# Kernel optimization log

Hardware: AMD Instinct MI355X
Metric: run time of the kernel (lower is better)

The kernel has to match this reference:

```python
import jax, jax.numpy as jnp
import numpy as np

N_NODES = 50000
N_EDGES = 1600000
IN_CH = 512
HID = 8      # per-head features, layer 1
HEADS = 8
OUT_CH = 40  # num classes
NEG_SLOPE = 0.2  # PyG GATConv default leaky_relu slope


def setup_inputs() -> dict:
    key = jax.random.key(0)
    ks = jax.random.split(key, 8)
    x = jax.random.uniform(ks[0], (N_NODES, IN_CH), dtype=jnp.float32)
    edge_index = jax.random.randint(ks[1], (2, N_EDGES), 0, N_NODES, dtype=jnp.int64)
    s1 = 1.0 / np.sqrt(IN_CH)
    s2 = 1.0 / np.sqrt(HEADS * HID)
    W1 = jax.random.normal(ks[2], (IN_CH, HEADS * HID), dtype=jnp.float32) * s1
    att_src1 = jax.random.normal(ks[3], (HEADS, HID), dtype=jnp.float32) * s2
    att_dst1 = jax.random.normal(ks[4], (HEADS, HID), dtype=jnp.float32) * s2
    b1 = jnp.zeros((HEADS * HID,), dtype=jnp.float32)
    W2 = jax.random.normal(ks[5], (HEADS * HID, OUT_CH), dtype=jnp.float32) * s2
    att_src2 = jax.random.normal(ks[6], (1, OUT_CH), dtype=jnp.float32) * 0.15
    att_dst2 = jax.random.normal(ks[7], (1, OUT_CH), dtype=jnp.float32) * 0.15
    b2 = jnp.zeros((OUT_CH,), dtype=jnp.float32)
    return {"x": x, "edge_index": edge_index, "W1": W1, "att_src1": att_src1,
            "att_dst1": att_dst1, "b1": b1, "W2": W2, "att_src2": att_src2,
            "att_dst2": att_dst2, "b2": b2}


def _row_normalize(x):
    return x / jnp.clip(x.sum(axis=1, keepdims=True), 1e-8, None)


def _gat_conv(x, src, dst, W, att_src, att_dst, bias, heads, out_ch, concat):
    """PyG GATConv (self-loops already included in src/dst)."""
    n = x.shape[0]
    h = (x @ W).reshape(n, heads, out_ch)          # [N, H, C]
    a_src = jnp.sum(h * att_src, axis=-1)          # [N, H]
    a_dst = jnp.sum(h * att_dst, axis=-1)          # [N, H]
    alpha = jax.nn.leaky_relu(a_src[src] + a_dst[dst], NEG_SLOPE)  # [E, H]
    # segment softmax over incoming edges of each dst node
    m = jax.ops.segment_max(alpha, dst, num_segments=n)            # [N, H]
    e = jnp.exp(alpha - m[dst])
    denom = jax.ops.segment_sum(e, dst, num_segments=n)            # [N, H]
    alpha = e / (denom[dst] + 1e-16)
    msg = h[src] * alpha[:, :, None]               # [E, H, C]
    out = jax.ops.segment_sum(msg, dst, num_segments=n)            # [N, H, C]
    out = out.reshape(n, heads * out_ch) if concat else out.mean(axis=1)
    return out + bias


def reference(x, edge_index, W1, att_src1, att_dst1, b1, W2, att_src2, att_dst2, b2):
    n = x.shape[0]
    loops = jnp.arange(n, dtype=edge_index.dtype)
    src = jnp.concatenate([edge_index[0], loops])
    dst = jnp.concatenate([edge_index[1], loops])
    h = _row_normalize(x)
    # dropout omitted: inference mode (training=False)
    h = jax.nn.elu(_gat_conv(h, src, dst, W1, att_src1, att_dst1, b1, HEADS, HID, True))
    return _gat_conv(h, src, dst, W2, att_src2, att_dst2, b2, 1, OUT_CH, False)
```

## Files before the change

### kernel.cpp

```cpp
#include <hip/hip_runtime.h>
#include <math.h>

#define N_NODES 50000
#define IN_CH   512
#define HID     8
#define HEADS   8
#define C1      64
#define OUT_CH  40
#define NEG_SLOPE 0.2f
#define NB      ((N_NODES + 255) / 256)
#define TILE    4096
#define CAP     16384

__device__ __forceinline__ float leaky(float v) { return fmaxf(v, NEG_SLOPE * v); }
__device__ __forceinline__ float fexp(float v) { return __expf(v); }

typedef __attribute__((ext_vector_type(8))) short short8;
typedef __attribute__((ext_vector_type(4))) short short4v;
typedef __attribute__((ext_vector_type(4))) float f32x4;

__device__ __forceinline__ unsigned short f2bf(float f) {
    unsigned u = __builtin_bit_cast(unsigned, f);
    u += 0x7FFFu + ((u >> 16) & 1u);
    return (unsigned short)(u >> 16);
}
__device__ __forceinline__ float bf2f(unsigned short h) {
    unsigned u = ((unsigned)h) << 16;
    return __builtin_bit_cast(float, u);
}

#define XH_STRIDE_B 272

__global__ __launch_bounds__(256) void k_packW(
    const float* __restrict__ W1, short* __restrict__ bph, short* __restrict__ bpl)
{
    const int idx = blockIdx.x * 256 + threadIdx.x;
    if (idx >= 512 * 64) return;
    const int k = idx >> 6, col = idx & 63;
    const float w = W1[idx];
    const unsigned short hi = f2bf(w);
    const unsigned short lo = f2bf(w - bf2f(hi));
    const int di = ((k >> 5) * 64 + col) * 32 + (k & 31);
    bph[di] = (short)hi;
    bpl[di] = (short)lo;
}

__global__ __launch_bounds__(256) void k_gemm1_mfma(
    const float* __restrict__ x,
    const short* __restrict__ bph, const short* __restrict__ bpl,
    const float* __restrict__ attS, const float* __restrict__ attD,
    unsigned short* __restrict__ h1b, float* __restrict__ aS, float* __restrict__ aD)
{
    __shared__ unsigned char smem[17536];
    short* xh = (short*)smem;
    short* xl = (short*)(smem + 8704);
    float* rowsum = (float*)(smem + 17408);
    float* houtf  = (float*)smem;

    const int tid  = threadIdx.x;
    const int lane = tid & 63;
    const int w    = tid >> 6;
    const int row_off = (w & 1) * 16;
    const int col_off = (w >> 1) * 32;
    const int rowBase = blockIdx.x * 32;

    const int l15 = lane & 15;
    const int kg  = lane >> 4;
    const int a_base = (l15 + row_off) * XH_STRIDE_B + kg * 16;

    const int srow = tid >> 5;
    const int sk4  = tid & 31;

    f32x4 acc0 = {0.f, 0.f, 0.f, 0.f};
    f32x4 acc1 = {0.f, 0.f, 0.f, 0.f};
    float psum[4] = {0.f, 0.f, 0.f, 0.f};
    float4 va[4], vb[4];

    auto LOAD = [&](int c, float4 (&v)[4]) {
        #pragma unroll
        for (int i = 0; i < 4; ++i) {
            const int grow = rowBase + i * 8 + srow;
            v[i] = (grow < N_NODES)
                 ? *(const float4*)(x + (size_t)grow * IN_CH + c * 128 + sk4 * 4)
                 : make_float4(0.f, 0.f, 0.f, 0.f);
        }
    };
    auto STAGE = [&](float4 (&v)[4]) {
        #pragma unroll
        for (int i = 0; i < 4; ++i) {
            const int row = i * 8 + srow;
            const unsigned short h0 = f2bf(v[i].x), h1u = f2bf(v[i].y),
                                 h2 = f2bf(v[i].z), h3  = f2bf(v[i].w);
            short4v hvv = { (short)h0, (short)h1u, (short)h2, (short)h3 };
            short4v lvv = { (short)f2bf(v[i].x - bf2f(h0)), (short)f2bf(v[i].y - bf2f(h1u)),
                            (short)f2bf(v[i].z - bf2f(h2)), (short)f2bf(v[i].w - bf2f(h3)) };
            *(short4v*)((char*)xh + row * XH_STRIDE_B + sk4 * 8) = hvv;
            *(short4v*)((char*)xl + row * XH_STRIDE_B + sk4 * 8) = lvv;
            psum[i] += v[i].x + v[i].y + v[i].z + v[i].w;
        }
    };
    auto MFMA = [&](int c) {
        #pragma unroll
        for (int kk2 = 0; kk2 < 4; ++kk2) {
            const int kk = c * 4 + kk2;
            const short8 ah = *(const short8*)((const char*)xh + a_base + kk2 * 64);
            const short8 al = *(const short8*)((const char*)xl + a_base + kk2 * 64);
            const int b0 = (kk * 64 + col_off + l15) * 32 + kg * 8;
            const int b1 = b0 + 16 * 32;
            const short8 bh0 = *(const short8*)(bph + b0);
            const short8 bl0 = *(const short8*)(bpl + b0);
            const short8 bh1 = *(const short8*)(bph + b1);
            const short8 bl1 = *(const short8*)(bpl + b1);
            acc0 = __builtin_amdgcn_mfma_f32_16x16x32_bf16(ah, bh0, acc0, 0, 0, 0);
            acc1 = __builtin_amdgcn_mfma_f32_16x16x32_bf16(ah, bh1, acc1, 0, 0, 0);
            acc0 = __builtin_amdgcn_mfma_f32_16x16x32_bf16(ah, bl0, acc0, 0, 0, 0);
            acc1 = __builtin_amdgcn_mfma_f32_16x16x32_bf16(ah, bl1, acc1, 0, 0, 0);
            acc0 = __builtin_amdgcn_mfma_f32_16x16x32_bf16(al, bh0, acc0, 0, 0, 0);
            acc1 = __builtin_amdgcn_mfma_f32_16x16x32_bf16(al, bh1, acc1, 0, 0, 0);
        }
    };

    LOAD(0, va);
    STAGE(va);
    __syncthreads();
    LOAD(1, vb);
    MFMA(0);
    __syncthreads();
    STAGE(vb);
    __syncthreads();
    LOAD(2, va);
    MFMA(1);
    __syncthreads();
    STAGE(va);
    __syncthreads();
    LOAD(3, vb);
    MFMA(2);
    __syncthreads();
    STAGE(vb);
    #pragma unroll
    for (int i = 0; i < 4; ++i) {
        float s = psum[i];
        #pragma unroll
        for (int off = 16; off; off >>= 1) s += __shfl_xor(s, off, 32);
        if (sk4 == 0) rowsum[i * 8 + srow] = s;
    }
    __syncthreads();
    MFMA(3);
    __syncthreads();

    #pragma unroll
    for (int r = 0; r < 4; ++r) {
        const int row = row_off + kg * 4 + r;
        const float rs = fmaxf(rowsum[row], 1e-8f);
        houtf[row * 68 + col_off + l15]      = acc0[r] / rs;
        houtf[row * 68 + col_off + 16 + l15] = acc1[r] / rs;
    }
    __syncthreads();

    #pragma unroll
    for (int i = tid; i < 32 * 16; i += 256) {
        const int row = i >> 4, seg = i & 15;
        if (rowBase + row < N_NODES) {
            const float* hs = houtf + row * 68 + seg * 4;
            short4v o = { (short)f2bf(hs[0]), (short)f2bf(hs[1]),
                          (short)f2bf(hs[2]), (short)f2bf(hs[3]) };
            *(short4v*)(h1b + (size_t)(rowBase + row) * 64 + seg * 4) = o;
        }
    }

    {
        const int row = tid >> 3, hd = tid & 7;
        if (rowBase + row < N_NODES) {
            float vs = 0.f, vd = 0.f;
            #pragma unroll
            for (int e2 = 0; e2 < 8; ++e2) {
                const float hv = houtf[row * 68 + hd * 8 + e2];
                vs = fmaf(hv, attS[hd * 8 + e2], vs);
                vd = fmaf(hv, attD[hd * 8 + e2], vd);
            }
            aS[(size_t)(rowBase + row) * 8 + hd] = vs;
            aD[(size_t)(rowBase + row) * 8 + hd] = vd;
        }
    }
}

__global__ __launch_bounds__(256) void k_initCur(int* __restrict__ coarseCur)
{
    const int t = threadIdx.x;
    if (t < NB) coarseCur[t] = t * CAP;
}

__global__ __launch_bounds__(256) void k_part(
    const int* __restrict__ src, const int* __restrict__ dst, int E,
    int* __restrict__ coarseCur, unsigned int* __restrict__ pairs)
{
    __shared__ int  hist[256];
    __shared__ int  scn[256];
    __shared__ int  offs[256];
    __shared__ unsigned int  pairBuf[TILE];
    __shared__ unsigned char bktBuf[TILE];

    const int t = threadIdx.x;
    const int tileBase = blockIdx.x * TILE;
    const int n = min(TILE, E - tileBase);

    hist[t] = 0;
    __syncthreads();

    for (int e = t; e < n; e += 256)
        atomicAdd(&hist[dst[tileBase + e] >> 8], 1);
    __syncthreads();

    scn[t] = hist[t];
    __syncthreads();
    #pragma unroll
    for (int off = 1; off < 256; off <<= 1) {
        int xv = (t >= off) ? scn[t - off] : 0;
        __syncthreads();
        scn[t] += xv;
        __syncthreads();
    }

    {
        const int h  = hist[t];
        const int ls = scn[t] - h;
        int off = 0;
        if (h > 0) {
            const int gbase = atomicAdd(&coarseCur[t], h);
            off = gbase - ls;
        }
        offs[t] = off;
        hist[t] = ls;
    }
    __syncthreads();

    for (int e = t; e < n; e += 256) {
        const int s = src[tileBase + e];
        const int d = dst[tileBase + e];
        const int bkt = d >> 8;
        const int pos = atomicAdd(&hist[bkt], 1);
        pairBuf[pos] = (unsigned)s | ((unsigned)(d & 255) << 17);
        bktBuf[pos]  = (unsigned char)bkt;
    }
    __syncthreads();

    for (int i = t; i < n; i += 256)
        pairs[i + offs[bktBuf[i]]] = pairBuf[i];
}

__global__ __launch_bounds__(256) void k_fine2(
    const int* __restrict__ coarseCur,
    const unsigned int* __restrict__ pairs, int* __restrict__ ssrc,
    int* __restrict__ cumS, int* __restrict__ cumE)
{
    __shared__ int hist[256];
    __shared__ int scn[256];
    __shared__ int cur[256];
    const int b = blockIdx.x;
    const int t = threadIdx.x;
    const int dbase = b << 8;
    const int nd = min(256, N_NODES - dbase);
    const int lo = b * CAP;
    const int hi = coarseCur[b];

    hist[t] = 0;
    __syncthreads();
    for (int j = lo + t; j < hi; j += 256)
        atomicAdd(&hist[(pairs[j] >> 17) & 255], 1);
    __syncthreads();

    const int hv = hist[t];
    scn[t] = hv;
    __syncthreads();
    #pragma unroll
    for (int off = 1; off < 256; off <<= 1) {
        int xv = (t >= off) ? scn[t - off] : 0;
        __syncthreads();
        scn[t] += xv;
        __syncthreads();
    }
    if (t < nd) {
        cumS[dbase + t] = lo + scn[t] - hv;
        cumE[dbase + t] = lo + scn[t];
    }
    cur[t] = lo + scn[t] - hv;
    __syncthreads();

    for (int j = lo + t; j < hi; j += 256) {
        const unsigned int p = pairs[j];
        const int pos = atomicAdd(&cur[(p >> 17) & 255], 1);
        ssrc[pos] = (int)(p & 0x1FFFFu);
    }
}

__global__ __launch_bounds__(256) void k_agg1f(
    const int* __restrict__ cumS, const int* __restrict__ cumE,
    const int* __restrict__ ssrc,
    const float* __restrict__ aS, const float* __restrict__ aD,
    const unsigned short* __restrict__ h1b, const float* __restrict__ b1,
    const float* __restrict__ W2,
    const float* __restrict__ attS2, const float* __restrict__ attD2,
    unsigned short* __restrict__ h2b, float* __restrict__ a2s, float* __restrict__ a2d)
{
    __shared__ float w2s[64 * 40];
    __shared__ float hstage[4][64];

    const int tid  = threadIdx.x;
    const int lane = tid & 63;
    const int w    = tid >> 6;
    const int node = __builtin_amdgcn_readfirstlane(blockIdx.x * 4 + w);
    const int e = lane >> 3;
    const int c = lane & 7;

    #pragma unroll
    for (int i = tid; i < 640; i += 256)
        ((float4*)w2s)[i] = ((const float4*)W2)[i];

    const int start = cumS[node];
    const int end   = cumE[node];

    const float aDn = aD[(size_t)node * 8 + c];
    float acc[8] = {0.f, 0.f, 0.f, 0.f, 0.f, 0.f, 0.f, 0.f};
    float den = 0.f;

    if (e == 0) {
        const float e0 = fexp(leaky(aS[(size_t)node * 8 + c] + aDn));
        const short8 hv = *(const short8*)(h1b + (size_t)node * 64 + c * 8);
        #pragma unroll
        for (int j = 0; j < 8; ++j)
            acc[j] = e0 * bf2f((unsigned short)hv[j]);
        den = e0;
    }

    int base = start;
    for (; base + 32 <= end; base += 32) {
        const int s0 = ssrc[base + e];
        const int s1 = ssrc[base + 8 + e];
        const int s2 = ssrc[base + 16 + e];
        const int s3 = ssrc[base + 24 + e];
        const float aa0 = aS[(size_t)s0 * 8 + c];
        const float aa1 = aS[(size_t)s1 * 8 + c];
        const float aa2 = aS[(size_t)s2 * 8 + c];
        const float aa3 = aS[(size_t)s3 * 8 + c];
        const short8 h0 = *(const short8*)(h1b + ((size_t)s0 << 6) + c * 8);
        const short8 h1v = *(const short8*)(h1b + ((size_t)s1 << 6) + c * 8);
        const short8 h2v = *(const short8*)(h1b + ((size_t)s2 << 6) + c * 8);
        const short8 h3v = *(const short8*)(h1b + ((size_t)s3 << 6) + c * 8);
        const float w0 = fexp(leaky(aa0 + aDn));
        const float w1 = fexp(leaky(aa1 + aDn));
        const float w2 = fexp(leaky(aa2 + aDn));
        const float w3 = fexp(leaky(aa3 + aDn));
        #pragma unroll
        for (int j = 0; j < 8; ++j) {
            acc[j] = fmaf(w0, bf2f((unsigned short)h0[j]), acc[j]);
            acc[j] = fmaf(w1, bf2f((unsigned short)h1v[j]), acc[j]);
            acc[j] = fmaf(w2, bf2f((unsigned short)h2v[j]), acc[j]);
            acc[j] = fmaf(w3, bf2f((unsigned short)h3v[j]), acc[j]);
        }
        den += w0 + w1 + w2 + w3;
    }
    for (; base + 8 <= end; base += 8) {
        const int s = ssrc[base + e];
        const float aa = aS[(size_t)s * 8 + c];
        const short8 hv = *(const short8*)(h1b + ((size_t)s << 6) + c * 8);
        const float wv = fexp(leaky(aa + aDn));
        #pragma unroll
        for (int j = 0; j < 8; ++j)
            acc[j] = fmaf(wv, bf2f((unsigned short)hv[j]), acc[j]);
        den += wv;
    }
    if (base < end) {
        const int nb  = end - base;
        const int idx = base + (e < nb ? e : nb - 1);
        const int s   = ssrc[idx];
        float wv = fexp(leaky(aS[(size_t)s * 8 + c] + aDn));
        if (e >= nb) wv = 0.f;
        const short8 hv = *(const short8*)(h1b + ((size_t)s << 6) + c * 8);
        #pragma unroll
        for (int j = 0; j < 8; ++j)
            acc[j] = fmaf(wv, bf2f((unsigned short)hv[j]), acc[j]);
        den += wv;
    }

    #pragma unroll
    for (int m = 8; m < 64; m <<= 1) {
        den += __shfl_xor(den, m, 64);
        #pragma unroll
        for (int j = 0; j < 8; ++j)
            acc[j] += __shfl_xor(acc[j], m, 64);
    }

    if (e == 0) {
        const float dinv = 1.f / (den + 1e-16f);
        #pragma unroll
        for (int j = 0; j < 8; ++j) {
            const float v = acc[j] * dinv + b1[c * 8 + j];
            hstage[w][c * 8 + j] = v > 0.f ? v : (__expf(v) - 1.f);
        }
    }
    __syncthreads();

    const int j = lane;
    float acc2 = 0.f;
    if (j < OUT_CH) {
        #pragma unroll
        for (int k = 0; k < 64; ++k)
            acc2 = fmaf(hstage[w][k], w2s[k * 40 + j], acc2);
    }
    float vs = (j < OUT_CH) ? acc2 * attS2[j] : 0.f;
    float vd = (j < OUT_CH) ? acc2 * attD2[j] : 0.f;
    #pragma unroll
    for (int off = 32; off; off >>= 1) {
        vs += __shfl_xor(vs, off, 64);
        vd += __shfl_xor(vd, off, 64);
    }
    if (j < OUT_CH) h2b[(size_t)node * 40 + j] = f2bf(acc2);
    if (j == 0) {
        a2s[node] = vs;
        a2d[node] = vd;
    }
}

__global__ __launch_bounds__(256) void k_agg2(
    const int* __restrict__ cumS, const int* __restrict__ cumE,
    const int* __restrict__ ssrc,
    const float* __restrict__ a2s, const float* __restrict__ a2d,
    const unsigned short* __restrict__ h2b, const float* __restrict__ b2,
    float* __restrict__ out)
{
    const int lane = threadIdx.x & 63;
    const int node = __builtin_amdgcn_readfirstlane(blockIdx.x * 4 + (threadIdx.x >> 6));
    const int e = lane >> 3;
    const int c = lane & 7;

    const int start = cumS[node];
    const int end   = cumE[node];

    const float aDd = a2d[node];
    float acc[8] = {0.f, 0.f, 0.f, 0.f, 0.f, 0.f, 0.f, 0.f};
    float den = 0.f;

    if (e == 0) {
        const float e0 = fexp(leaky(a2s[node] + aDd));
        const short8 hv = *(const short8*)(h2b + (size_t)node * 40 + c * 8);
        #pragma unroll
        for (int j = 0; j < 8; ++j)
            acc[j] = e0 * bf2f((unsigned short)hv[j]);
        den = e0;
    }

    int base = start;
    for (; base + 32 <= end; base += 32) {
        const int s0 = ssrc[base + e];
        const int s1 = ssrc[base + 8 + e];
        const int s2 = ssrc[base + 16 + e];
        const int s3 = ssrc[base + 24 + e];
        const float aa0 = a2s[s0];
        const float aa1 = a2s[s1];
        const float aa2 = a2s[s2];
        const float aa3 = a2s[s3];
        const short8 h0 = *(const short8*)(h2b + (size_t)s0 * 40 + c * 8);
        const short8 h1v = *(const short8*)(h2b + (size_t)s1 * 40 + c * 8);
        const short8 h2v = *(const short8*)(h2b + (size_t)s2 * 40 + c * 8);
        const short8 h3v = *(const short8*)(h2b + (size_t)s3 * 40 + c * 8);
        const float w0 = fexp(leaky(aa0 + aDd));
        const float w1 = fexp(leaky(aa1 + aDd));
        const float w2 = fexp(leaky(aa2 + aDd));
        const float w3 = fexp(leaky(aa3 + aDd));
        #pragma unroll
        for (int j = 0; j < 8; ++j) {
            acc[j] = fmaf(w0, bf2f((unsigned short)h0[j]), acc[j]);
            acc[j] = fmaf(w1, bf2f((unsigned short)h1v[j]), acc[j]);
            acc[j] = fmaf(w2, bf2f((unsigned short)h2v[j]), acc[j]);
            acc[j] = fmaf(w3, bf2f((unsigned short)h3v[j]), acc[j]);
        }
        den += w0 + w1 + w2 + w3;
    }
    for (; base + 8 <= end; base += 8) {
        const int s = ssrc[base + e];
        const float aa = a2s[s];
        const short8 hv = *(const short8*)(h2b + (size_t)s * 40 + c * 8);
        const float wv = fexp(leaky(aa + aDd));
        #pragma unroll
        for (int j = 0; j < 8; ++j)
            acc[j] = fmaf(wv, bf2f((unsigned short)hv[j]), acc[j]);
        den += wv;
    }
    if (base < end) {
        const int nb  = end - base;
        const int idx = base + (e < nb ? e : nb - 1);
        const int s   = ssrc[idx];
        float wv = fexp(leaky(a2s[s] + aDd));
        if (e >= nb) wv = 0.f;
        const short8 hv = *(const short8*)(h2b + (size_t)s * 40 + c * 8);
        #pragma unroll
        for (int j = 0; j < 8; ++j)
            acc[j] = fmaf(wv, bf2f((unsigned short)hv[j]), acc[j]);
        den += wv;
    }

    #pragma unroll
    for (int m = 8; m < 64; m <<= 1) {
        den += __shfl_xor(den, m, 64);
        #pragma unroll
        for (int j = 0; j < 8; ++j)
            acc[j] += __shfl_xor(acc[j], m, 64);
    }

    if (e == 0 && c < 5) {
        const float dinv = 1.f / (den + 1e-16f);
        float o[8];
        #pragma unroll
        for (int j = 0; j < 8; ++j)
            o[j] = acc[j] * dinv + b2[c * 8 + j];
        float4* dst0 = (float4*)(out + (size_t)node * OUT_CH + c * 8);
        dst0[0] = make_float4(o[0], o[1], o[2], o[3]);
        dst0[1] = make_float4(o[4], o[5], o[6], o[7]);
    }
}

extern "C" void kernel_launch(void* const* d_in, const int* in_sizes, int n_in,
                              void* d_out, int out_size, void* d_ws, size_t ws_size,
                              hipStream_t stream)
{
    const float* x     = (const float*)d_in[0];
    const int*   ei    = (const int*)d_in[1];
    const float* W1    = (const float*)d_in[2];
    const float* attS1 = (const float*)d_in[3];
    const float* attD1 = (const float*)d_in[4];
    const float* b1    = (const float*)d_in[5];
    const float* W2    = (const float*)d_in[6];
    const float* attS2 = (const float*)d_in[7];
    const float* attD2 = (const float*)d_in[8];
    const float* b2    = (const float*)d_in[9];

    const int E = in_sizes[1] / 2;
    const int* src = ei;
    const int* dst = ei + E;

    float* out = (float*)d_out;
    float* f = (float*)d_ws;
    float* aS1  = f;  f += (size_t)N_NODES * 8;
    float* aD1  = f;  f += (size_t)N_NODES * 8;
    float* a2s  = f;  f += (size_t)N_NODES;
    float* a2d  = f;  f += (size_t)N_NODES;
    unsigned short* h1b = (unsigned short*)f;  f += (size_t)N_NODES * 32;
    unsigned short* h2b = (unsigned short*)f;  f += (size_t)N_NODES * 20 + 64;
    short* bph = (short*)f;  f += 16384;
    short* bpl = (short*)f;  f += 16384;
    unsigned int* pairs = (unsigned int*)f;  f += (size_t)NB * CAP;
    int* ip = (int*)f;
    int* coarseCur = ip;  ip += 256;
    int* cumS      = ip;  ip += N_NODES;
    int* cumE      = ip;  ip += N_NODES;
    int* ssrc      = ip;  ip += (size_t)NB * CAP;

    const int partBlocks = (E + TILE - 1) / TILE;

    k_initCur<<<1, 256, 0, stream>>>(coarseCur);
    k_part<<<partBlocks, 256, 0, stream>>>(src, dst, E, coarseCur, pairs);
    k_fine2<<<NB, 256, 0, stream>>>(coarseCur, pairs, ssrc, cumS, cumE);

    k_packW<<<(512 * 64 + 255) / 256, 256, 0, stream>>>(W1, bph, bpl);
    k_gemm1_mfma<<<(N_NODES + 31) / 32, 256, 0, stream>>>(x, bph, bpl, attS1, attD1,
                                                          h1b, aS1, aD1);
    k_agg1f<<<N_NODES / 4, 256, 0, stream>>>(cumS, cumE, ssrc, aS1, aD1, h1b, b1,
                                             W2, attS2, attD2, h2b, a2s, a2d);

    k_agg2<<<N_NODES / 4, 256, 0, stream>>>(cumS, cumE, ssrc, a2s, a2d, h2b, b2, out);
}
```

Measured before the change: 179.8 us.

## Enlarge partition tile, transpose W2 in LDS, drop block barrier, skip dead lanes

Doubles the edge-partition tile to 8192 edges per block, so fewer blocks do the coarse bucketing with more shared memory each. In the fused layer-1 aggregation, W2 is stored transposed and padded in LDS so each lane can do vectorized float4 dot products, and the post-aggregation block barrier becomes a wave-local barrier. That is valid because each wave reads only its own hstage row, but a block barrier is now needed after the W2 fill. In layer-2 aggregation, lanes with c>=5 no longer load or accumulate the out-of-range bf16 feature columns, which cuts redundant gathers.

```diff
diff --git a/kernel.cpp b/kernel.cpp
--- a/kernel.cpp
+++ b/kernel.cpp
@@ -9,7 +9,7 @@
 #define OUT_CH  40
 #define NEG_SLOPE 0.2f
 #define NB      ((N_NODES + 255) / 256)
-#define TILE    4096
+#define PART_TILE 8192
 #define CAP     16384
 
 __device__ __forceinline__ float leaky(float v) { return fmaxf(v, NEG_SLOPE * v); }
@@ -197,12 +197,12 @@
     __shared__ int  hist[256];
     __shared__ int  scn[256];
     __shared__ int  offs[256];
-    __shared__ unsigned int  pairBuf[TILE];
-    __shared__ unsigned char bktBuf[TILE];
+    __shared__ unsigned int  pairBuf[PART_TILE];
+    __shared__ unsigned char bktBuf[PART_TILE];
 
     const int t = threadIdx.x;
-    const int tileBase = blockIdx.x * TILE;
-    const int n = min(TILE, E - tileBase);
+    const int tileBase = blockIdx.x * PART_TILE;
+    const int n = min(PART_TILE, E - tileBase);
 
     hist[t] = 0;
     __syncthreads();
@@ -302,7 +302,7 @@
     const float* __restrict__ attS2, const float* __restrict__ attD2,
     unsigned short* __restrict__ h2b, float* __restrict__ a2s, float* __restrict__ a2d)
 {
-    __shared__ float w2s[64 * 40];
+    __shared__ float w2sT[40 * 68];
     __shared__ float hstage[4][64];
 
     const int tid  = threadIdx.x;
@@ -312,9 +312,11 @@
     const int e = lane >> 3;
     const int c = lane & 7;
 
-    #pragma unroll
-    for (int i = tid; i < 640; i += 256)
-        ((float4*)w2s)[i] = ((const float4*)W2)[i];
+    for (int i = tid; i < 2560; i += 256) {
+        const int k = i / 40, j = i - k * 40;
+        w2sT[j * 68 + k] = W2[i];
+    }
+    __syncthreads();
 
     const int start = cumS[node];
     const int end   = cumE[node];
@@ -398,14 +400,22 @@
             hstage[w][c * 8 + j] = v > 0.f ? v : (__expf(v) - 1.f);
         }
     }
-    __syncthreads();
+    asm volatile("s_waitcnt lgkmcnt(0)" ::: "memory");
+    __builtin_amdgcn_wave_barrier();
+    __builtin_amdgcn_sched_barrier(0);
 
     const int j = lane;
     float acc2 = 0.f;
     if (j < OUT_CH) {
         #pragma unroll
-        for (int k = 0; k < 64; ++k)
-            acc2 = fmaf(hstage[w][k], w2s[k * 40 + j], acc2);
+        for (int k4 = 0; k4 < 16; ++k4) {
+            const f32x4 hv4 = *(const f32x4*)(&hstage[w][k4 * 4]);
+            const f32x4 wv4 = *(const f32x4*)(&w2sT[j * 68 + k4 * 4]);
+            acc2 = fmaf(hv4.x, wv4.x, acc2);
+            acc2 = fmaf(hv4.y, wv4.y, acc2);
+            acc2 = fmaf(hv4.z, wv4.z, acc2);
+            acc2 = fmaf(hv4.w, wv4.w, acc2);
+        }
     }
     float vs = (j < OUT_CH) ? acc2 * attS2[j] : 0.f;
     float vd = (j < OUT_CH) ? acc2 * attD2[j] : 0.f;
@@ -442,10 +452,12 @@
 
     if (e == 0) {
         const float e0 = fexp(leaky(a2s[node] + aDd));
-        const short8 hv = *(const short8*)(h2b + (size_t)node * 40 + c * 8);
-        #pragma unroll
-        for (int j = 0; j < 8; ++j)
-            acc[j] = e0 * bf2f((unsigned short)hv[j]);
+        if (c < 5) {
+            const short8 hv = *(const short8*)(h2b + (size_t)node * 40 + c * 8);
+            #pragma unroll
+            for (int j = 0; j < 8; ++j)
+                acc[j] = e0 * bf2f((unsigned short)hv[j]);
+        }
         den = e0;
     }
 
@@ -459,31 +471,39 @@
         const float aa1 = a2s[s1];
         const float aa2 = a2s[s2];
         const float aa3 = a2s[s3];
-        const short8 h0 = *(const short8*)(h2b + (size_t)s0 * 40 + c * 8);
-        const short8 h1v = *(const short8*)(h2b + (size_t)s1 * 40 + c * 8);
-        const short8 h2v = *(const short8*)(h2b + (size_t)s2 * 40 + c * 8);
-        const short8 h3v = *(const short8*)(h2b + (size_t)s3 * 40 + c * 8);
+        short8 h0 = {0,0,0,0,0,0,0,0}, h1v = {0,0,0,0,0,0,0,0};
+        short8 h2v = {0,0,0,0,0,0,0,0}, h3v = {0,0,0,0,0,0,0,0};
+        if (c < 5) {
+            h0  = *(const short8*)(h2b + (size_t)s0 * 40 + c * 8);
+            h1v = *(const short8*)(h2b + (size_t)s1 * 40 + c * 8);
+            h2v = *(const short8*)(h2b + (size_t)s2 * 40 + c * 8);
+            h3v = *(const short8*)(h2b + (size_t)s3 * 40 + c * 8);
+        }
         const float w0 = fexp(leaky(aa0 + aDd));
         const float w1 = fexp(leaky(aa1 + aDd));
         const float w2 = fexp(leaky(aa2 + aDd));
         const float w3 = fexp(leaky(aa3 + aDd));
-        #pragma unroll
-        for (int j = 0; j < 8; ++j) {
-            acc[j] = fmaf(w0, bf2f((unsigned short)h0[j]), acc[j]);
-            acc[j] = fmaf(w1, bf2f((unsigned short)h1v[j]), acc[j]);
-            acc[j] = fmaf(w2, bf2f((unsigned short)h2v[j]), acc[j]);
-            acc[j] = fmaf(w3, bf2f((unsigned short)h3v[j]), acc[j]);
+        if (c < 5) {
+            #pragma unroll
+            for (int j = 0; j < 8; ++j) {
+                acc[j] = fmaf(w0, bf2f((unsigned short)h0[j]), acc[j]);
+                acc[j] = fmaf(w1, bf2f((unsigned short)h1v[j]), acc[j]);
+                acc[j] = fmaf(w2, bf2f((unsigned short)h2v[j]), acc[j]);
+                acc[j] = fmaf(w3, bf2f((unsigned short)h3v[j]), acc[j]);
+            }
         }
         den += w0 + w1 + w2 + w3;
     }
     for (; base + 8 <= end; base += 8) {
         const int s = ssrc[base + e];
         const float aa = a2s[s];
-        const short8 hv = *(const short8*)(h2b + (size_t)s * 40 + c * 8);
         const float wv = fexp(leaky(aa + aDd));
-        #pragma unroll
-        for (int j = 0; j < 8; ++j)
-            acc[j] = fmaf(wv, bf2f((unsigned short)hv[j]), acc[j]);
+        if (c < 5) {
+            const short8 hv = *(const short8*)(h2b + (size_t)s * 40 + c * 8);
+            #pragma unroll
+            for (int j = 0; j < 8; ++j)
+                acc[j] = fmaf(wv, bf2f((unsigned short)hv[j]), acc[j]);
+        }
         den += wv;
     }
     if (base < end) {
@@ -492,10 +512,12 @@
         const int s   = ssrc[idx];
         float wv = fexp(leaky(a2s[s] + aDd));
         if (e >= nb) wv = 0.f;
-        const short8 hv = *(const short8*)(h2b + (size_t)s * 40 + c * 8);
-        #pragma unroll
-        for (int j = 0; j < 8; ++j)
-            acc[j] = fmaf(wv, bf2f((unsigned short)hv[j]), acc[j]);
+        if (c < 5) {
+            const short8 hv = *(const short8*)(h2b + (size_t)s * 40 + c * 8);
+            #pragma unroll
+            for (int j = 0; j < 8; ++j)
+                acc[j] = fmaf(wv, bf2f((unsigned short)hv[j]), acc[j]);
+        }
         den += wv;
     }
 
@@ -555,7 +577,7 @@
     int* cumE      = ip;  ip += N_NODES;
     int* ssrc      = ip;  ip += (size_t)NB * CAP;
 
-    const int partBlocks = (E + TILE - 1) / TILE;
+    const int partBlocks = (E + PART_TILE - 1) / PART_TILE;
 
     k_initCur<<<1, 256, 0, stream>>>(coarseCur);
     k_part<<<partBlocks, 256, 0, stream>>>(src, dst, E, coarseCur, pairs);
```

Result: slower. 191.1 us (+6.3%).
